# Performance work log

Measured on AMD Instinct MI355X. Metric: run time of the kernel, lower is better.

The kernel has to match this reference:

```python
import jax, jax.numpy as jnp
import numpy as np

B, U, D = 128, 200, 512

def setup_inputs() -> dict:
    key = jax.random.key(0)
    k1, k2, k3 = jax.random.split(key, 3)
    input_real = jax.random.normal(k1, (B, D, D), dtype=jnp.float32)
    input_imag = jax.random.normal(k2, (B, D, D), dtype=jnp.float32)
    # keras 'uniform' initializer: U(-0.05, 0.05); unit_norm constraint normalizes over axes (1,2)
    kernel = jax.random.uniform(k3, (U, D, 2), dtype=jnp.float32, minval=-0.05, maxval=0.05)
    kernel = kernel / jnp.linalg.norm(kernel.reshape(U, -1), axis=1)[:, None, None]
    return {"input_real": input_real, "input_imag": input_imag, "kernel": kernel}

def reference(input_real, input_imag, kernel):
    # kernel: [U, D, 2] -> real/imag measurement vectors
    kr = kernel[:, :, 0]  # [U, D]
    ki = kernel[:, :, 1]  # [U, D]
    # Original: M_real = kr kr^T - ki ki^T ; M_imag = ki kr^T + kr ki^T (outer products per unit)
    # out[b,n] = trace(R_b @ M_real_n) - trace(I_b @ M_imag_n)
    # trace(A @ (u v^T)) = sum_ij A[i,j] u[j] v[i] -> quadratic form, avoids [B,U,D,D] tiles.
    t_real = (jnp.einsum('bij,nj,ni->bn', input_real, kr, kr)
              - jnp.einsum('bij,nj,ni->bn', input_real, ki, ki))
    t_imag = (jnp.einsum('bij,nj,ni->bn', input_imag, ki, kr)
              + jnp.einsum('bij,nj,ni->bn', input_imag, kr, ki))
    return t_real - t_imag  # [B, U]
```

## Files before the change

kernel.cpp:

```cpp
#include <hip/hip_runtime.h>
#include <hip/hip_bf16.h>
#include <string.h>

#define BB 128
#define UU 200
#define DD 512
#define NP 256
#define NWS 504

typedef __attribute__((ext_vector_type(8))) short short8;
typedef __attribute__((ext_vector_type(4))) float f32x4;

__device__ __forceinline__ unsigned pack_bf16_2(float a, float b) {
    __hip_bfloat162 h = __float22bfloat162_rn(make_float2(a, b));
    unsigned u; memcpy(&u, &h, 4); return u;
}

__device__ __forceinline__ unsigned short f2bf(float x) {
    union { float f; unsigned u; } v; v.f = x;
    unsigned r = v.u + 0x7FFFu + ((v.u >> 16) & 1u);
    return (unsigned short)(r >> 16);
}

__global__ void kb_build_kernel(const float* __restrict__ Kt, unsigned* __restrict__ Kb) {
    int idx = blockIdx.x * 256 + threadIdx.x;
    int n = idx >> 9, j = idx & 511;
    unsigned v = 0u;
    if (n < UU) {
        float2 s = ((const float2*)Kt)[(size_t)n * DD + j];
        v = pack_bf16_2(s.x, s.y);
    }
    Kb[idx] = v;
}

__global__ void zero_out_kernel(float* __restrict__ out) {
    int i = blockIdx.x * 256 + threadIdx.x;
    if (i < BB * UU) out[i] = 0.0f;
}

__global__ void reduce_kernel(const float* __restrict__ ws, float* __restrict__ out) {
    int o = blockIdx.x * 256 + threadIdx.x;
    if (o >= BB * UU) return;
    int p0 = blockIdx.y * 36;
    float s = 0.0f;
#pragma unroll
    for (int p = 0; p < 36; ++p)
        s += ws[(size_t)(p0 + p) * (BB * UU) + o];
    atomicAdd(&out[o], s);
}

__global__ __launch_bounds__(1024, 4) void cm_gemm2_kernel(
    const float* __restrict__ Ar, const float* __restrict__ Ai,
    const float* __restrict__ Kt, const unsigned* __restrict__ Kb,
    float* __restrict__ ws, float* __restrict__ out)
{
    __shared__ short sA[2 * 128 * 128];

    const int tid  = threadIdx.x;
    const int irow = blockIdx.x;
    const int w    = tid >> 6;
    const int lane = tid & 63;
    const int rrow = lane & 15;
    const int quad = lane >> 4;
    const int nn   = w * 16 + rrow;
    const int xr   = rrow & 7;

    float krI = 0.f, kiI = 0.f;
    if (nn < UU) {
        float2 s = ((const float2*)Kt)[(size_t)nn * DD + irow];
        krI = s.x; kiI = s.y;
    }
    const float nkrI = -krI, nkiI = -kiI;

    const int g = tid & 31, r0 = tid >> 5;
    unsigned boff[4];
    int waddr[4];
#pragma unroll
    for (int l = 0; l < 4; ++l) {
        int row = r0 + 32 * l;
        boff[l] = (unsigned)row * (DD * DD) + (unsigned)irow * DD + g * 4;
        waddr[l] = row * 128 + (((g >> 1) ^ (row & 7)) * 8) + (g & 1) * 4;
    }

    f32x4 acc[8];
#pragma unroll
    for (int t = 0; t < 8; ++t) acc[t] = (f32x4)(0.f);

    f32x4 pf[4];
#pragma unroll
    for (int l = 0; l < 4; ++l) pf[l] = *(const f32x4*)(Ar + boff[l]);

    short8 bi_sv[4];

    for (int t = 0; t < 8; ++t) {
        const int ph = t & 1;
        const int j0 = (t >> 1) * 128;
        short* sb = &sA[(t & 1) * (128 * 128)];

#pragma unroll
        for (int l = 0; l < 4; ++l) {
            uint2 u;
            u.x = pack_bf16_2(pf[l][0], pf[l][1]);
            u.y = pack_bf16_2(pf[l][2], pf[l][3]);
            *(uint2*)&sb[waddr[l]] = u;
        }
        __syncthreads();

        if (t < 7) {
            const int tn = t + 1;
            const float* P = (tn & 1) ? Ai : Ar;
            const unsigned jn = (unsigned)((tn >> 1) * 128);
#pragma unroll
            for (int l = 0; l < 4; ++l) pf[l] = *(const f32x4*)(P + boff[l] + jn);
        }

        const unsigned* kbp = Kb + (unsigned)nn * DD + j0 + quad * 8;
        uint4 nx0, nx1;
        if (ph == 0) { nx0 = *(const uint4*)kbp; nx1 = *(const uint4*)(kbp + 4); }

#pragma unroll
        for (int kk = 0; kk < 4; ++kk) {
            short8 bfrag;
            if (ph == 0) {
                uint4 c0 = nx0, c1 = nx1;
                if (kk < 3) {
                    nx0 = *(const uint4*)(kbp + (kk + 1) * 32);
                    nx1 = *(const uint4*)(kbp + (kk + 1) * 32 + 4);
                }
                unsigned dw[8] = {c0.x, c0.y, c0.z, c0.w, c1.x, c1.y, c1.z, c1.w};
                float wr[8], wi[8];
#pragma unroll
                for (int e = 0; e < 8; ++e) {
                    union { unsigned u; float f; } a, b;
                    a.u = dw[e] << 16;
                    b.u = dw[e] & 0xFFFF0000u;
                    wr[e] = krI * a.f + nkiI * b.f;
                    wi[e] = nkrI * b.f + nkiI * a.f;
                }
                union { short8 v; unsigned u[4]; } pr, pi;
#pragma unroll
                for (int e = 0; e < 4; ++e) {
                    pr.u[e] = pack_bf16_2(wr[2 * e], wr[2 * e + 1]);
                    pi.u[e] = pack_bf16_2(wi[2 * e], wi[2 * e + 1]);
                }
                bfrag = pr.v;
                bi_sv[kk] = pi.v;
            } else {
                bfrag = bi_sv[kk];
            }

#pragma unroll
            for (int h = 0; h < 2; ++h) {
                short8 af[4];
#pragma unroll
                for (int q = 0; q < 4; ++q) {
                    int row = (h * 4 + q) * 16 + rrow;
                    int gran = (kk * 4 + quad) ^ xr;
                    af[q] = *(const short8*)&sb[row * 128 + gran * 8];
                }
#pragma unroll
                for (int q = 0; q < 4; ++q)
                    acc[h * 4 + q] = __builtin_amdgcn_mfma_f32_16x16x32_bf16(
                        af[q], bfrag, acc[h * 4 + q], 0, 0, 0);
            }
        }
    }

    if (nn < UU) {
        if (irow < NWS) {
            float* wsp = ws + (size_t)irow * (BB * UU);
#pragma unroll
            for (int ti = 0; ti < 8; ++ti) {
                int m = ti * 16 + quad * 4;
#pragma unroll
                for (int r = 0; r < 4; ++r)
                    wsp[(size_t)(m + r) * UU + nn] = acc[ti][r];
            }
        } else {
#pragma unroll
            for (int ti = 0; ti < 8; ++ti) {
                int m = ti * 16 + quad * 4;
#pragma unroll
                for (int r = 0; r < 4; ++r)
                    atomicAdd(&out[(size_t)(m + r) * UU + nn], acc[ti][r]);
            }
        }
    }
}

#define ASTR 40
#define WSTR 40
__global__ __launch_bounds__(512, 4) void cm_gemm_fb_kernel(
    const float* __restrict__ Ar, const float* __restrict__ Ai,
    const float* __restrict__ Kt, float* __restrict__ dst)
{
    __shared__ short sAr[BB * ASTR];
    __shared__ short sAi[BB * ASTR];
    __shared__ short sWr[NP * WSTR];
    __shared__ short sWi[NP * WSTR];
    const int tid = threadIdx.x, irow = blockIdx.x;
    const int w = tid >> 6, lane = tid & 63;
    const int mw = (w & 1) * 64, nw = (w >> 1) * 64;
    const int rrow = lane & 15, quad = lane >> 4;
    const int nW = tid >> 1, jh = (tid & 1) * 16;
    float krI = 0.f, kiI = 0.f;
    if (nW < UU) { float2 s = ((const float2*)Kt)[(size_t)nW * DD + irow]; krI = s.x; kiI = s.y; }
    const int brow0 = tid >> 3, grp = tid & 7;
    const size_t aoff0 = (size_t)brow0 * DD * DD + (size_t)irow * DD + (size_t)grp * 4;
    const size_t aoff1 = aoff0 + (size_t)64 * DD * DD;
    f32x4 acc[4][4];
#pragma unroll
    for (int a = 0; a < 4; ++a)
#pragma unroll
        for (int b = 0; b < 4; ++b) acc[a][b] = (f32x4)(0.f);
    for (int jw = 0; jw < DD; jw += 32) {
        f32x4 vr0 = *(const f32x4*)(Ar + aoff0 + jw);
        f32x4 vr1 = *(const f32x4*)(Ar + aoff1 + jw);
        f32x4 vi0 = *(const f32x4*)(Ai + aoff0 + jw);
        f32x4 vi1 = *(const f32x4*)(Ai + aoff1 + jw);
        union { unsigned short s[4]; uint2 u; } t0, t1, t2, t3;
#pragma unroll
        for (int q = 0; q < 4; ++q) {
            t0.s[q] = f2bf(vr0[q]); t1.s[q] = f2bf(vr1[q]);
            t2.s[q] = f2bf(vi0[q]); t3.s[q] = f2bf(vi1[q]);
        }
        *(uint2*)&sAr[ brow0       * ASTR + grp * 4] = t0.u;
        *(uint2*)&sAr[(brow0 + 64) * ASTR + grp * 4] = t1.u;
        *(uint2*)&sAi[ brow0       * ASTR + grp * 4] = t2.u;
        *(uint2*)&sAi[(brow0 + 64) * ASTR + grp * 4] = t3.u;
        if (nW < UU) {
            const f32x4* kv = (const f32x4*)(Kt + (size_t)nW * DD * 2 + (size_t)(jw + jh) * 2);
#pragma unroll
            for (int q = 0; q < 8; ++q) {
                f32x4 v = kv[q];
                float wr0 = krI * v[0] - kiI * v[1], wi0 = -(krI * v[1] + kiI * v[0]);
                float wr1 = krI * v[2] - kiI * v[3], wi1 = -(krI * v[3] + kiI * v[2]);
                *(unsigned*)&sWr[nW * WSTR + jh + 2 * q] = (unsigned)f2bf(wr0) | ((unsigned)f2bf(wr1) << 16);
                *(unsigned*)&sWi[nW * WSTR + jh + 2 * q] = (unsigned)f2bf(wi0) | ((unsigned)f2bf(wi1) << 16);
            }
        } else {
#pragma unroll
            for (int q = 0; q < 8; ++q) {
                *(unsigned*)&sWr[nW * WSTR + jh + 2 * q] = 0u;
                *(unsigned*)&sWi[nW * WSTR + jh + 2 * q] = 0u;
            }
        }
        __syncthreads();
#pragma unroll
        for (int ph = 0; ph < 2; ++ph) {
            const short* sA = ph ? sAi : sAr;
            const short* sW = ph ? sWi : sWr;
            short8 af[4], bf[4];
#pragma unroll
            for (int t = 0; t < 4; ++t) {
                af[t] = *(const short8*)&sA[(mw + t * 16 + rrow) * ASTR + quad * 8];
                bf[t] = *(const short8*)&sW[(nw + t * 16 + rrow) * WSTR + quad * 8];
            }
#pragma unroll
            for (int ti = 0; ti < 4; ++ti)
#pragma unroll
                for (int tj = 0; tj < 4; ++tj)
                    acc[ti][tj] = __builtin_amdgcn_mfma_f32_16x16x32_bf16(af[ti], bf[tj], acc[ti][tj], 0, 0, 0);
        }
        __syncthreads();
    }
#pragma unroll
    for (int ti = 0; ti < 4; ++ti) {
        int m = mw + ti * 16 + quad * 4;
#pragma unroll
        for (int tj = 0; tj < 4; ++tj) {
            int n = nw + tj * 16 + rrow;
            if (n < UU)
#pragma unroll
                for (int r = 0; r < 4; ++r)
                    atomicAdd(&dst[(size_t)(m + r) * UU + n], acc[ti][tj][r]);
        }
    }
}

extern "C" void kernel_launch(void* const* d_in, const int* in_sizes, int n_in,
                              void* d_out, int out_size, void* d_ws, size_t ws_size,
                              hipStream_t stream) {
    const float* Ar = (const float*)d_in[0];
    const float* Ai = (const float*)d_in[1];
    const float* Kt = (const float*)d_in[2];
    float* out = (float*)d_out;

    const size_t kb_dwords = (size_t)NP * DD;
    const size_t ws_need = kb_dwords * 4 + (size_t)NWS * BB * UU * 4;

    if (ws_size >= ws_need) {
        unsigned* Kb = (unsigned*)d_ws;
        float* ws = (float*)d_ws + kb_dwords;
        hipLaunchKernelGGL(kb_build_kernel, dim3(512), dim3(256), 0, stream, Kt, Kb);
        hipLaunchKernelGGL(zero_out_kernel, dim3(100), dim3(256), 0, stream, out);
        hipLaunchKernelGGL(cm_gemm2_kernel, dim3(DD), dim3(1024), 0, stream,
                           Ar, Ai, Kt, Kb, ws, out);
        hipLaunchKernelGGL(reduce_kernel, dim3(100, 14), dim3(256), 0, stream, ws, out);
    } else {
        hipLaunchKernelGGL(zero_out_kernel, dim3(100), dim3(256), 0, stream, out);
        hipLaunchKernelGGL(cm_gemm_fb_kernel, dim3(DD), dim3(512), 0, stream, Ar, Ai, Kt, out);
    }
}
```

Measured before the change: 306.5 us.

## Restructure quadratic form as per-batch complex GEMM with fused epilogue reduction

The main kernel is reorganised so each block handles one batch and a 64-row slice of i. It computes complex products A·k over all j with MFMAs using the precomputed bf16 real and imaginary kernel vectors, then contracts against k_i in the epilogue with shuffles and one atomic per unit. This removes the large workspace, the separate reduce kernel and the per-irow scaled weight construction, and the output zeroing is folded into the build kernel. In exchange the MFMA count doubles, since four complex products are needed per A fragment, and atomics to out now come from eight blocks per batch.

```diff
diff --git a/kernel.cpp b/kernel.cpp
--- a/kernel.cpp
+++ b/kernel.cpp
@@ -6,7 +6,6 @@
 #define UU 200
 #define DD 512
 #define NP 256
-#define NWS 504
 
 typedef __attribute__((ext_vector_type(8))) short short8;
 typedef __attribute__((ext_vector_type(4))) float f32x4;
@@ -22,15 +21,20 @@
     return (unsigned short)(r >> 16);
 }
 
-__global__ void kb_build_kernel(const float* __restrict__ Kt, unsigned* __restrict__ Kb) {
+__global__ void kb2_build_kernel(const float* __restrict__ Kt,
+                                 unsigned short* __restrict__ Kbr,
+                                 unsigned short* __restrict__ Kbi,
+                                 float* __restrict__ out) {
     int idx = blockIdx.x * 256 + threadIdx.x;
     int n = idx >> 9, j = idx & 511;
-    unsigned v = 0u;
+    unsigned short r = 0, im = 0;
     if (n < UU) {
         float2 s = ((const float2*)Kt)[(size_t)n * DD + j];
-        v = pack_bf16_2(s.x, s.y);
-    }
-    Kb[idx] = v;
+        r = f2bf(s.x); im = f2bf(s.y);
+    }
+    Kbr[idx] = r;
+    Kbi[idx] = im;
+    if (idx < BB * UU) out[idx] = 0.0f;
 }
 
 __global__ void zero_out_kernel(float* __restrict__ out) {
@@ -38,153 +42,142 @@
     if (i < BB * UU) out[i] = 0.0f;
 }
 
-__global__ void reduce_kernel(const float* __restrict__ ws, float* __restrict__ out) {
-    int o = blockIdx.x * 256 + threadIdx.x;
-    if (o >= BB * UU) return;
-    int p0 = blockIdx.y * 36;
-    float s = 0.0f;
-#pragma unroll
-    for (int p = 0; p < 36; ++p)
-        s += ws[(size_t)(p0 + p) * (BB * UU) + o];
-    atomicAdd(&out[o], s);
-}
-
-__global__ __launch_bounds__(1024, 4) void cm_gemm2_kernel(
+__global__ __launch_bounds__(512, 4) void qf_gemm_kernel(
     const float* __restrict__ Ar, const float* __restrict__ Ai,
-    const float* __restrict__ Kt, const unsigned* __restrict__ Kb,
-    float* __restrict__ ws, float* __restrict__ out)
+    const float* __restrict__ Kt,
+    const unsigned short* __restrict__ Kbr, const unsigned short* __restrict__ Kbi,
+    float* __restrict__ out)
 {
-    __shared__ short sA[2 * 128 * 128];
+    __shared__ short sA[2][2][64 * 64];
 
     const int tid  = threadIdx.x;
-    const int irow = blockIdx.x;
+    const int bx   = blockIdx.x;
+    const int b    = bx >> 3;
+    const int i0   = (bx & 7) * 64;
+
     const int w    = tid >> 6;
     const int lane = tid & 63;
     const int rrow = lane & 15;
     const int quad = lane >> 4;
-    const int nn   = w * 16 + rrow;
     const int xr   = rrow & 7;
-
-    float krI = 0.f, kiI = 0.f;
-    if (nn < UU) {
-        float2 s = ((const float2*)Kt)[(size_t)nn * DD + irow];
-        krI = s.x; kiI = s.y;
-    }
-    const float nkrI = -krI, nkiI = -kiI;
-
-    const int g = tid & 31, r0 = tid >> 5;
-    unsigned boff[4];
-    int waddr[4];
-#pragma unroll
-    for (int l = 0; l < 4; ++l) {
+    const int nn0  = w * 32 + rrow;
+    const int nn1  = nn0 + 16;
+
+    const int g  = tid & 15;
+    const int r0 = tid >> 4;
+    const float* ArB = Ar + ((size_t)b * DD + i0) * DD;
+    const float* AiB = Ai + ((size_t)b * DD + i0) * DD;
+    unsigned aoff[2];
+    int waddr[2];
+#pragma unroll
+    for (int l = 0; l < 2; ++l) {
         int row = r0 + 32 * l;
-        boff[l] = (unsigned)row * (DD * DD) + (unsigned)irow * DD + g * 4;
-        waddr[l] = row * 128 + (((g >> 1) ^ (row & 7)) * 8) + (g & 1) * 4;
-    }
-
-    f32x4 acc[8];
-#pragma unroll
-    for (int t = 0; t < 8; ++t) acc[t] = (f32x4)(0.f);
+        aoff[l]  = (unsigned)row * DD + (unsigned)g * 4;
+        waddr[l] = row * 64 + (((g >> 1) ^ (row & 7)) * 8) + (g & 1) * 4;
+    }
+
+    const int rb0 = rrow * 64 + ((quad ^ xr)) * 8;
+    const int rb1 = rrow * 64 + ((quad ^ xr) ^ 4) * 8;
+
+    f32x4 accr[4][2], acci[4][2];
+#pragma unroll
+    for (int m = 0; m < 4; ++m)
+#pragma unroll
+        for (int nt = 0; nt < 2; ++nt) { accr[m][nt] = (f32x4)(0.f); acci[m][nt] = (f32x4)(0.f); }
 
     f32x4 pf[4];
-#pragma unroll
-    for (int l = 0; l < 4; ++l) pf[l] = *(const f32x4*)(Ar + boff[l]);
-
-    short8 bi_sv[4];
-
-    for (int t = 0; t < 8; ++t) {
-        const int ph = t & 1;
-        const int j0 = (t >> 1) * 128;
-        short* sb = &sA[(t & 1) * (128 * 128)];
-
-#pragma unroll
-        for (int l = 0; l < 4; ++l) {
-            uint2 u;
+    pf[0] = *(const f32x4*)(ArB + aoff[0]);
+    pf[1] = *(const f32x4*)(ArB + aoff[1]);
+    pf[2] = *(const f32x4*)(AiB + aoff[0]);
+    pf[3] = *(const f32x4*)(AiB + aoff[1]);
+
+#pragma unroll 2
+    for (int ss = 0; ss < 8; ++ss) {
+        short* bufR = &sA[ss & 1][0][0];
+        short* bufI = &sA[ss & 1][1][0];
+
+#pragma unroll
+        for (int l = 0; l < 2; ++l) {
+            uint2 u, v;
             u.x = pack_bf16_2(pf[l][0], pf[l][1]);
             u.y = pack_bf16_2(pf[l][2], pf[l][3]);
-            *(uint2*)&sb[waddr[l]] = u;
+            v.x = pack_bf16_2(pf[2 + l][0], pf[2 + l][1]);
+            v.y = pack_bf16_2(pf[2 + l][2], pf[2 + l][3]);
+            *(uint2*)&bufR[waddr[l]] = u;
+            *(uint2*)&bufI[waddr[l]] = v;
         }
         __syncthreads();
 
-        if (t < 7) {
-            const int tn = t + 1;
-            const float* P = (tn & 1) ? Ai : Ar;
-            const unsigned jn = (unsigned)((tn >> 1) * 128);
-#pragma unroll
-            for (int l = 0; l < 4; ++l) pf[l] = *(const f32x4*)(P + boff[l] + jn);
-        }
-
-        const unsigned* kbp = Kb + (unsigned)nn * DD + j0 + quad * 8;
-        uint4 nx0, nx1;
-        if (ph == 0) { nx0 = *(const uint4*)kbp; nx1 = *(const uint4*)(kbp + 4); }
-
-#pragma unroll
-        for (int kk = 0; kk < 4; ++kk) {
-            short8 bfrag;
-            if (ph == 0) {
-                uint4 c0 = nx0, c1 = nx1;
-                if (kk < 3) {
-                    nx0 = *(const uint4*)(kbp + (kk + 1) * 32);
-                    nx1 = *(const uint4*)(kbp + (kk + 1) * 32 + 4);
-                }
-                unsigned dw[8] = {c0.x, c0.y, c0.z, c0.w, c1.x, c1.y, c1.z, c1.w};
-                float wr[8], wi[8];
-#pragma unroll
-                for (int e = 0; e < 8; ++e) {
-                    union { unsigned u; float f; } a, b;
-                    a.u = dw[e] << 16;
-                    b.u = dw[e] & 0xFFFF0000u;
-                    wr[e] = krI * a.f + nkiI * b.f;
-                    wi[e] = nkrI * b.f + nkiI * a.f;
-                }
-                union { short8 v; unsigned u[4]; } pr, pi;
-#pragma unroll
-                for (int e = 0; e < 4; ++e) {
-                    pr.u[e] = pack_bf16_2(wr[2 * e], wr[2 * e + 1]);
-                    pi.u[e] = pack_bf16_2(wi[2 * e], wi[2 * e + 1]);
-                }
-                bfrag = pr.v;
-                bi_sv[kk] = pi.v;
-            } else {
-                bfrag = bi_sv[kk];
-            }
-
-#pragma unroll
-            for (int h = 0; h < 2; ++h) {
-                short8 af[4];
-#pragma unroll
-                for (int q = 0; q < 4; ++q) {
-                    int row = (h * 4 + q) * 16 + rrow;
-                    int gran = (kk * 4 + quad) ^ xr;
-                    af[q] = *(const short8*)&sb[row * 128 + gran * 8];
-                }
-#pragma unroll
-                for (int q = 0; q < 4; ++q)
-                    acc[h * 4 + q] = __builtin_amdgcn_mfma_f32_16x16x32_bf16(
-                        af[q], bfrag, acc[h * 4 + q], 0, 0, 0);
-            }
-        }
-    }
-
-    if (nn < UU) {
-        if (irow < NWS) {
-            float* wsp = ws + (size_t)irow * (BB * UU);
-#pragma unroll
-            for (int ti = 0; ti < 8; ++ti) {
-                int m = ti * 16 + quad * 4;
-#pragma unroll
-                for (int r = 0; r < 4; ++r)
-                    wsp[(size_t)(m + r) * UU + nn] = acc[ti][r];
-            }
-        } else {
-#pragma unroll
-            for (int ti = 0; ti < 8; ++ti) {
-                int m = ti * 16 + quad * 4;
-#pragma unroll
-                for (int r = 0; r < 4; ++r)
-                    atomicAdd(&out[(size_t)(m + r) * UU + nn], acc[ti][r]);
-            }
-        }
+        if (ss < 7) {
+            const unsigned jn = (unsigned)(ss + 1) * 64;
+            pf[0] = *(const f32x4*)(ArB + aoff[0] + jn);
+            pf[1] = *(const f32x4*)(ArB + aoff[1] + jn);
+            pf[2] = *(const f32x4*)(AiB + aoff[0] + jn);
+            pf[3] = *(const f32x4*)(AiB + aoff[1] + jn);
+        }
+
+        const int jbase = ss * 64;
+#pragma unroll
+        for (int kk = 0; kk < 2; ++kk) {
+            const int j = jbase + kk * 32 + quad * 8;
+            short8 bkr0 = *(const short8*)(Kbr + (size_t)nn0 * 512 + j);
+            short8 bkr1 = *(const short8*)(Kbr + (size_t)nn1 * 512 + j);
+            short8 bki0 = *(const short8*)(Kbi + (size_t)nn0 * 512 + j);
+            short8 bki1 = *(const short8*)(Kbi + (size_t)nn1 * 512 + j);
+            const int rb = kk ? rb1 : rb0;
+
+            short8 afR[4];
+#pragma unroll
+            for (int m = 0; m < 4; ++m)
+                afR[m] = *(const short8*)&bufR[rb + m * 1024];
+#pragma unroll
+            for (int m = 0; m < 4; ++m) {
+                accr[m][0] = __builtin_amdgcn_mfma_f32_16x16x32_bf16(afR[m], bkr0, accr[m][0], 0, 0, 0);
+                accr[m][1] = __builtin_amdgcn_mfma_f32_16x16x32_bf16(afR[m], bkr1, accr[m][1], 0, 0, 0);
+                acci[m][0] = __builtin_amdgcn_mfma_f32_16x16x32_bf16(afR[m], bki0, acci[m][0], 0, 0, 0);
+                acci[m][1] = __builtin_amdgcn_mfma_f32_16x16x32_bf16(afR[m], bki1, acci[m][1], 0, 0, 0);
+            }
+
+            union { short8 v; unsigned u[4]; } t0, t1;
+            t0.v = bki0; t1.v = bki1;
+#pragma unroll
+            for (int e = 0; e < 4; ++e) { t0.u[e] ^= 0x80008000u; t1.u[e] ^= 0x80008000u; }
+
+            short8 afI[4];
+#pragma unroll
+            for (int m = 0; m < 4; ++m)
+                afI[m] = *(const short8*)&bufI[rb + m * 1024];
+#pragma unroll
+            for (int m = 0; m < 4; ++m) {
+                accr[m][0] = __builtin_amdgcn_mfma_f32_16x16x32_bf16(afI[m], t0.v, accr[m][0], 0, 0, 0);
+                accr[m][1] = __builtin_amdgcn_mfma_f32_16x16x32_bf16(afI[m], t1.v, accr[m][1], 0, 0, 0);
+                acci[m][0] = __builtin_amdgcn_mfma_f32_16x16x32_bf16(afI[m], bkr0, acci[m][0], 0, 0, 0);
+                acci[m][1] = __builtin_amdgcn_mfma_f32_16x16x32_bf16(afI[m], bkr1, acci[m][1], 0, 0, 0);
+            }
+        }
+    }
+
+    float* outB = out + (size_t)b * UU;
+#pragma unroll
+    for (int nt = 0; nt < 2; ++nt) {
+        const int n = w * 32 + nt * 16 + rrow;
+        float s = 0.f;
+        if (n < UU) {
+            const float* kp = Kt + ((size_t)n * DD + i0 + quad * 4) * 2;
+#pragma unroll
+            for (int m = 0; m < 4; ++m) {
+                f32x4 k01 = *(const f32x4*)(kp + m * 32);
+                f32x4 k23 = *(const f32x4*)(kp + m * 32 + 4);
+                s += accr[m][nt][0] * k01[0] - acci[m][nt][0] * k01[1];
+                s += accr[m][nt][1] * k01[2] - acci[m][nt][1] * k01[3];
+                s += accr[m][nt][2] * k23[0] - acci[m][nt][2] * k23[1];
+                s += accr[m][nt][3] * k23[2] - acci[m][nt][3] * k23[3];
+            }
+        }
+        s += __shfl_xor(s, 16, 64);
+        s += __shfl_xor(s, 32, 64);
+        if (quad == 0 && n < UU)
+            atomicAdd(&outB[n], s);
     }
 }
 
@@ -212,7 +205,7 @@
 #pragma unroll
     for (int a = 0; a < 4; ++a)
 #pragma unroll
-        for (int b = 0; b < 4; ++b) acc[a][b] = (f32x4)(0.f);
+        for (int c = 0; c < 4; ++c) acc[a][c] = (f32x4)(0.f);
     for (int jw = 0; jw < DD; jw += 32) {
         f32x4 vr0 = *(const f32x4*)(Ar + aoff0 + jw);
         f32x4 vr1 = *(const f32x4*)(Ar + aoff1 + jw);
@@ -286,17 +279,14 @@
     const float* Kt = (const float*)d_in[2];
     float* out = (float*)d_out;
 
-    const size_t kb_dwords = (size_t)NP * DD;
-    const size_t ws_need = kb_dwords * 4 + (size_t)NWS * BB * UU * 4;
-
-    if (ws_size >= ws_need) {
-        unsigned* Kb = (unsigned*)d_ws;
-        float* ws = (float*)d_ws + kb_dwords;
-        hipLaunchKernelGGL(kb_build_kernel, dim3(512), dim3(256), 0, stream, Kt, Kb);
-        hipLaunchKernelGGL(zero_out_kernel, dim3(100), dim3(256), 0, stream, out);
-        hipLaunchKernelGGL(cm_gemm2_kernel, dim3(DD), dim3(1024), 0, stream,
-                           Ar, Ai, Kt, Kb, ws, out);
-        hipLaunchKernelGGL(reduce_kernel, dim3(100, 14), dim3(256), 0, stream, ws, out);
+    const size_t kb_need = (size_t)2 * NP * DD * sizeof(unsigned short);
+
+    if (ws_size >= kb_need) {
+        unsigned short* Kbr = (unsigned short*)d_ws;
+        unsigned short* Kbi = Kbr + (size_t)NP * DD;
+        hipLaunchKernelGGL(kb2_build_kernel, dim3(512), dim3(256), 0, stream, Kt, Kbr, Kbi, out);
+        hipLaunchKernelGGL(qf_gemm_kernel, dim3(1024), dim3(512), 0, stream,
+                           Ar, Ai, Kt, Kbr, Kbi, out);
     } else {
         hipLaunchKernelGGL(zero_out_kernel, dim3(100), dim3(256), 0, stream, out);
         hipLaunchKernelGGL(cm_gemm_fb_kernel, dim3(DD), dim3(512), 0, stream, Ar, Ai, Kt, out);
```

Measured after the change: 387.0 us. 1.26x slower.
